# Kernel tuning notes

Measured on AMD Instinct MI355X. Metric: run time of the kernel, lower is better.

## Reference

```python
import jax, jax.numpy as jnp
import numpy as np

N_HEADS = 12

def setup_inputs() -> dict:
    key = jax.random.key(0)
    ks = jax.random.split(key, 3)
    B, C, T = 4, 768, 2048
    x = jax.random.normal(ks[0], (B, C, T), dtype=jnp.float32)
    mask = jnp.ones((B, 1, 1, T), dtype=jnp.int32)  # all valid; masked_fill where mask==0
    Wqkv = jax.random.normal(ks[1], (3 * C, C), dtype=jnp.float32) * 0.02
    bqkv = jnp.zeros((3 * C,), dtype=jnp.float32)
    Wout = jax.random.normal(ks[2], (C, C), dtype=jnp.float32) * 0.02
    bout = jnp.zeros((C,), dtype=jnp.float32)
    return {"x": x, "mask": mask, "Wqkv": Wqkv, "bqkv": bqkv, "Wout": Wout, "bout": bout}


def reference(x, mask, Wqkv, bqkv, Wout, bout):
    B, C, T = x.shape
    H = N_HEADS
    d = C // H
    scale = 1.0 / jnp.sqrt(jnp.asarray(d, x.dtype))
    # 1x1 Conv1d == per-timestep matmul over channels
    qkv = jnp.einsum('oc,bct->bot', Wqkv, x) + bqkv[None, :, None]  # [B,3C,T]
    # channel dim splits as [3, H, d] per the torch view(B,3,H,d,T)
    qkv = qkv.reshape(B, 3, H, d, T).transpose(0, 1, 2, 4, 3)       # [B,3,H,T,d]
    q, k, v = qkv[:, 0], qkv[:, 1], qkv[:, 2]
    score = jnp.einsum('bhtd,bhsd->bhts', q, k) * scale             # [B,H,T,T]
    score = jnp.where(mask == 0, jnp.asarray(-10000.0, score.dtype), score)
    attn = jax.nn.softmax(score, axis=-1)  # dropout: eval mode (identity)
    o = jnp.einsum('bhts,bhsd->bhtd', attn, v)                      # [B,H,T,d]
    o = o.transpose(0, 1, 3, 2).reshape(B, C, T)                    # [B,C,T]
    return jnp.einsum('oc,bct->bot', Wout, o) + bout[None, :, None]
```

## Files before the change

kernel.cpp:

```cpp
#include <hip/hip_runtime.h>
#include <hip/hip_bf16.h>
#include <stdint.h>

#define B_   4
#define C_   768
#define T_   2048
#define H_   12
#define D_   64
#define O3_  2304

typedef __attribute__((ext_vector_type(4))) float f32x4;
typedef __attribute__((ext_vector_type(8))) short bf16x8;

__device__ __forceinline__ unsigned short f2bf(float f) {
  union { float f; unsigned int u; } v; v.f = f;
  unsigned int r = v.u + 0x7fffu + ((v.u >> 16) & 1u);
  return (unsigned short)(r >> 16);
}

__device__ __forceinline__ unsigned int pack2bf(float a, float b) {
  __hip_bfloat162 h2 = __float22bfloat162_rn(make_float2(a, b));
  union { __hip_bfloat162 h; unsigned int u; } cv; cv.h = h2;
  return cv.u;
}

__device__ __forceinline__ float fexp2(float x) {
#if __has_builtin(__builtin_amdgcn_exp2f)
  return __builtin_amdgcn_exp2f(x);
#else
  return exp2f(x);
#endif
}

__device__ __forceinline__ void async16(const void* g, void* lds) {
#if __has_builtin(__builtin_amdgcn_global_load_lds)
  __builtin_amdgcn_global_load_lds((const __attribute__((address_space(1))) void*)g,
                                   (__attribute__((address_space(3))) void*)lds, 16, 0, 0);
#else
  int lane = threadIdx.x & 63;
  *((uint4*)((char*)lds + lane * 16)) = *((const uint4*)g);
#endif
}


__global__ void cvt_f32_bf16(const float* __restrict__ in,
                             unsigned short* __restrict__ out, int n4) {
  int i = blockIdx.x * 256 + threadIdx.x;
  if (i < n4) {
    float4 f = ((const float4*)in)[i];
    ushort4 o;
    o.x = f2bf(f.x); o.y = f2bf(f.y); o.z = f2bf(f.z); o.w = f2bf(f.w);
    ((ushort4*)out)[i] = o;
  }
}

__global__ void make_bias(const int* __restrict__ mask, float* __restrict__ mbias, int n) {
  int i = blockIdx.x * 256 + threadIdx.x;
  if (i < n) mbias[i] = (mask[i] == 0) ? -14426.950408f : 0.0f;
}

__global__ void transpose_x(const float* __restrict__ x,
                            unsigned short* __restrict__ xT) {
  __shared__ unsigned short tile[32][33];
  int b = blockIdx.z;
  int c0 = blockIdx.y * 32;
  int t0 = blockIdx.x * 32;
  int tid = threadIdx.x;
  {
    int cl = tid >> 3;
    int tl = (tid & 7) * 4;
    float4 f = *(const float4*)(x + ((size_t)b * C_ + c0 + cl) * T_ + t0 + tl);
    tile[tl + 0][cl] = f2bf(f.x);
    tile[tl + 1][cl] = f2bf(f.y);
    tile[tl + 2][cl] = f2bf(f.z);
    tile[tl + 3][cl] = f2bf(f.w);
  }
  __syncthreads();
  {
    int tl = tid >> 3;
    int cl = (tid & 7) * 4;
    ushort4 o;
    o.x = tile[tl][cl + 0]; o.y = tile[tl][cl + 1];
    o.z = tile[tl][cl + 2]; o.w = tile[tl][cl + 3];
    *(ushort4*)(xT + ((size_t)b * T_ + t0 + tl) * C_ + c0 + cl) = o;
  }
}

__global__ __launch_bounds__(256, 3)
void gemm_qkv(const unsigned short* __restrict__ xT,
              const unsigned short* __restrict__ W1,
              const float* __restrict__ bqkv,
              unsigned short* __restrict__ Qb,
              unsigned short* __restrict__ Kb,
              unsigned short* __restrict__ Vb) {
  __shared__ unsigned short sA[3][128 * 32];
  __shared__ unsigned short sB[3][128 * 32];

  const int b   = blockIdx.z;
  const int o0  = blockIdx.y * 128;
  const int t0  = blockIdx.x * 128;
  const int tid = threadIdx.x;
  const int wave = tid >> 6, lane = tid & 63;
  const int q = lane >> 4, ln = lane & 15;
  const int tw = wave >> 1, ow = wave & 1;

  const unsigned short* Ax = xT + (size_t)b * T_ * C_;
  const int srow = lane >> 2;
  const int ssw  = ((lane >> 2) ^ (lane >> 4)) & 3;
  const int scol = ((lane & 3) ^ ssw) * 8;
  const int rsw  = (ln ^ (ln >> 2)) & 3;

  const f32x4 ZERO = {0.f, 0.f, 0.f, 0.f};
  f32x4 acc[4][4];
#pragma unroll
  for (int mi = 0; mi < 4; ++mi)
#pragma unroll
    for (int ni = 0; ni < 4; ++ni) acc[mi][ni] = ZERO;

  auto stageA = [&](int ks, int bufi) {
#pragma unroll
    for (int j = 0; j < 2; ++j) {
      const int chunk = wave * 2 + j;
      async16(Ax + (size_t)(t0 + chunk * 16 + srow) * C_ + ks * 32 + scol,
              &sA[bufi][chunk * 512]);
    }
  };
  auto stageB = [&](int ks, int bufi) {
#pragma unroll
    for (int j = 0; j < 2; ++j) {
      const int chunk = wave * 2 + j;
      async16(W1 + (size_t)(o0 + chunk * 16 + srow) * C_ + ks * 32 + scol,
              &sB[bufi][chunk * 512]);
    }
  };
  auto sync4 = [&]() {
    __builtin_amdgcn_sched_barrier(0);
    asm volatile("s_waitcnt vmcnt(4) lgkmcnt(0)" ::: "memory");
    __builtin_amdgcn_s_barrier();
    __builtin_amdgcn_sched_barrier(0);
  };
  auto sync0 = [&]() {
    __builtin_amdgcn_sched_barrier(0);
    asm volatile("s_waitcnt vmcnt(0) lgkmcnt(0)" ::: "memory");
    __builtin_amdgcn_s_barrier();
    __builtin_amdgcn_sched_barrier(0);
  };
  auto compute = [&](int bufi) {
    bf16x8 aF[4], bF[4];
#pragma unroll
    for (int mi = 0; mi < 4; ++mi)
      aF[mi] = *(const bf16x8*)(&sA[bufi][(tw * 64 + mi * 16 + ln) * 32 + ((q ^ rsw) << 3)]);
#pragma unroll
    for (int ni = 0; ni < 4; ++ni)
      bF[ni] = *(const bf16x8*)(&sB[bufi][(ow * 64 + ni * 16 + ln) * 32 + ((q ^ rsw) << 3)]);
#pragma unroll
    for (int mi = 0; mi < 4; ++mi)
#pragma unroll
      for (int ni = 0; ni < 4; ++ni)
        acc[mi][ni] = __builtin_amdgcn_mfma_f32_16x16x32_bf16(aF[mi], bF[ni], acc[mi][ni], 0, 0, 0);
  };

  stageA(0, 0); stageB(0, 0);
  stageA(1, 1); stageB(1, 1);

  for (int g = 0; g < 7; ++g) {
    const int t3 = g * 3;
    sync4(); stageA(t3 + 2, 2); stageB(t3 + 2, 2); compute(0);
    sync4(); stageA(t3 + 3, 0); stageB(t3 + 3, 0); compute(1);
    sync4(); stageA(t3 + 4, 1); stageB(t3 + 4, 1); compute(2);
  }
  sync4(); stageA(23, 2); stageB(23, 2); compute(0);
  sync4(); compute(1);
  sync0(); compute(2);

  const float QSCL = 0.125f * 1.44269504f;
#pragma unroll
  for (int ni = 0; ni < 4; ++ni) {
    const int o = o0 + ow * 64 + ni * 16 + ln;
    const float bias = bqkv[o];
    const int which = o / C_;
    const int rem = o - which * C_;
    const int bh = b * H_ + (rem >> 6);
    const int dd = rem & 63;
#pragma unroll
    for (int mi = 0; mi < 4; ++mi) {
      const int tb = t0 + tw * 64 + mi * 16 + q * 4;
      f32x4 v = acc[mi][ni];
      if (which == 0) {
#pragma unroll
        for (int r = 0; r < 4; ++r)
          Qb[((size_t)bh * T_ + tb + r) * D_ + dd] = f2bf((v[r] + bias) * QSCL);
      } else if (which == 1) {
#pragma unroll
        for (int r = 0; r < 4; ++r) {
          const int s = tb + r;
          const int cp = (dd >> 3) ^ (s & 7);
          Kb[((size_t)bh * T_ + s) * 64 + (cp << 3) + (dd & 7)] = f2bf(v[r] + bias);
        }
      } else {
        const int tile = tb >> 6, si = tb & 63;
        const int cp = (si >> 3) ^ (dd & 7);
        ushort4 pk;
        pk.x = f2bf(v[0] + bias);
        pk.y = f2bf(v[1] + bias);
        pk.z = f2bf(v[2] + bias);
        pk.w = f2bf(v[3] + bias);
        *(ushort4*)(Vb + (((size_t)bh * 32 + tile) * 64 + dd) * 64 + (cp << 3) + (si & 7)) = pk;
      }
    }
  }
}

__global__ __launch_bounds__(256, 3)
void attn(const unsigned short* __restrict__ Qb,
          const unsigned short* __restrict__ Kb,
          const unsigned short* __restrict__ Vb,
          const float* __restrict__ mbias,
          unsigned short* __restrict__ Ob) {
  __shared__ __align__(16) char smem[49152];
  unsigned short* sK0 = (unsigned short*)smem;
  unsigned short* sV0 = (unsigned short*)(smem + 24576);

  const int id = blockIdx.x;
  const int bh = id % 48;
  const int tblk = id / 48;
  const int b = bh / H_, h = bh % H_;
  const int tid = threadIdx.x, wave = tid >> 6, lane = tid & 63;
  const int q = lane >> 4, ln = lane & 15;
  const int t0w = tblk * 128 + wave * 32;

  bf16x8 Qa[2][2];
#pragma unroll
  for (int tt = 0; tt < 2; ++tt) {
    const unsigned short* qrow = Qb + ((size_t)bh * T_ + t0w + tt * 16 + ln) * D_;
    Qa[tt][0] = *(const bf16x8*)(qrow + q * 8);
    Qa[tt][1] = *(const bf16x8*)(qrow + 32 + q * 8);
  }

  const f32x4 ZERO = {0.f, 0.f, 0.f, 0.f};
  f32x4 Oacc[4][2];
  f32x4 lacc[2];
#pragma unroll
  for (int dt = 0; dt < 4; ++dt)
#pragma unroll
    for (int tt = 0; tt < 2; ++tt) Oacc[dt][tt] = ZERO;
#pragma unroll
  for (int tt = 0; tt < 2; ++tt) lacc[tt] = ZERO;

  const short one_s = (ln == 0) ? (short)0x3F80 : (short)0;
  bf16x8 ones;
#pragma unroll
  for (int j = 0; j < 8; ++j) ones[j] = one_s;

  const unsigned short* gK = Kb + (size_t)bh * T_ * 64;
  const unsigned short* gV = Vb + (size_t)bh * 32 * 4096;
  const float* mb = mbias + b * T_;

  unsigned int maskbits = 0;
  for (int t2 = 0; t2 < 32; ++t2)
    if (__ballot(mb[t2 * 64 + lane] != 0.0f) != 0ull) maskbits |= (1u << t2);

  auto stage = [&](const unsigned short* g, unsigned short* lds) {
#pragma unroll
    for (int j = 0; j < 2; ++j) {
      const int chunk = wave * 2 + j;
      async16(g + chunk * 512 + lane * 8, lds + chunk * 512);
    }
  };

  auto sync4 = [&]() {
    __builtin_amdgcn_sched_barrier(0);
    asm volatile("s_waitcnt vmcnt(4) lgkmcnt(0)" ::: "memory");
    __builtin_amdgcn_s_barrier();
    __builtin_amdgcn_sched_barrier(0);
  };
  auto sync0 = [&]() {
    __builtin_amdgcn_sched_barrier(0);
    asm volatile("s_waitcnt vmcnt(0) lgkmcnt(0)" ::: "memory");
    __builtin_amdgcn_s_barrier();
    __builtin_amdgcn_sched_barrier(0);
  };

  auto QK = [&](const unsigned short* sKc, int it, bf16x8 pfO[2][2]) {
    const int s0 = it * 64;
    const bool anymask = (maskbits >> it) & 1;
#pragma unroll
    for (int kc = 0; kc < 2; ++kc) {
      bf16x8 kf0[2], kf1[2];
#pragma unroll
      for (int sb = 0; sb < 2; ++sb) {
        const unsigned short* krow = sKc + (kc * 32 + sb * 16 + ln) * 64;
        kf0[sb] = *(const bf16x8*)(krow + ((q ^ (ln & 7)) << 3));
        kf1[sb] = *(const bf16x8*)(krow + (((4 + q) ^ (ln & 7)) << 3));
      }
#pragma unroll
      for (int tt = 0; tt < 2; ++tt) {
        f32x4 sc[2];
#pragma unroll
        for (int sb = 0; sb < 2; ++sb) {
          f32x4 p0 = __builtin_amdgcn_mfma_f32_16x16x32_bf16(kf0[sb], Qa[tt][0], ZERO, 0, 0, 0);
          sc[sb]   = __builtin_amdgcn_mfma_f32_16x16x32_bf16(kf1[sb], Qa[tt][1], p0, 0, 0, 0);
          if (anymask) {
            f32x4 bb = *(const f32x4*)(mb + s0 + kc * 32 + sb * 16 + q * 4);
#pragma unroll
            for (int r = 0; r < 4; ++r) sc[sb][r] += bb[r];
          }
        }
        unsigned int A0 = pack2bf(fexp2(sc[0][0]), fexp2(sc[0][1]));
        unsigned int B0 = pack2bf(fexp2(sc[0][2]), fexp2(sc[0][3]));
        unsigned int C0 = pack2bf(fexp2(sc[1][0]), fexp2(sc[1][1]));
        unsigned int E0 = pack2bf(fexp2(sc[1][2]), fexp2(sc[1][3]));
        asm volatile("v_permlane32_swap_b32 %0, %1" : "+v"(A0), "+v"(C0));
        asm volatile("v_permlane16_swap_b32 %0, %1" : "+v"(A0), "+v"(C0));
        asm volatile("v_permlane32_swap_b32 %0, %1" : "+v"(B0), "+v"(E0));
        asm volatile("v_permlane16_swap_b32 %0, %1" : "+v"(B0), "+v"(E0));
        union { bf16x8 v; unsigned int u[4]; } P;
        P.u[0] = A0;
        P.u[1] = B0;
        P.u[2] = C0;
        P.u[3] = E0;
        pfO[tt][kc] = P.v;
      }
    }
  };

  auto PV = [&](const unsigned short* sVc, bf16x8 pfI[2][2]) {
#pragma unroll
    for (int dt = 0; dt < 4; ++dt) {
#pragma unroll
      for (int kc = 0; kc < 2; ++kc) {
        bf16x8 vf = *(const bf16x8*)(sVc + (dt * 16 + ln) * 64 +
                                     (((kc * 4 + q) ^ (ln & 7)) << 3));
#pragma unroll
        for (int tt = 0; tt < 2; ++tt)
          Oacc[dt][tt] = __builtin_amdgcn_mfma_f32_16x16x32_bf16(vf, pfI[tt][kc], Oacc[dt][tt], 0, 0, 0);
      }
    }
#pragma unroll
    for (int kc = 0; kc < 2; ++kc)
#pragma unroll
      for (int tt = 0; tt < 2; ++tt)
        lacc[tt] = __builtin_amdgcn_mfma_f32_16x16x32_bf16(ones, pfI[tt][kc], lacc[tt], 0, 0, 0);
  };

  bf16x8 pf[2][2];

  stage(gK, sK0);
  stage(gV, sV0);
  stage(gK + 4096, sK0 + 4096);
  stage(gV + 4096, sV0 + 4096);

  for (int ith = 0; ith < 10; ++ith) {
    const int it = ith * 3;
    sync4();
    stage(gK + (size_t)(it + 2) * 4096, sK0 + 2 * 4096);
    stage(gV + (size_t)(it + 2) * 4096, sV0 + 2 * 4096);
    QK(sK0, it, pf);
    PV(sV0, pf);
    sync4();
    stage(gK + (size_t)(it + 3) * 4096, sK0);
    stage(gV + (size_t)(it + 3) * 4096, sV0);
    QK(sK0 + 4096, it + 1, pf);
    PV(sV0 + 4096, pf);
    sync4();
    stage(gK + (size_t)(it + 4) * 4096, sK0 + 4096);
    stage(gV + (size_t)(it + 4) * 4096, sV0 + 4096);
    QK(sK0 + 2 * 4096, it + 2, pf);
    PV(sV0 + 2 * 4096, pf);
  }

  sync4();
  QK(sK0, 30, pf);
  PV(sV0, pf);
  sync0();
  QK(sK0 + 4096, 31, pf);
  PV(sV0 + 4096, pf);

#pragma unroll
  for (int tt = 0; tt < 2; ++tt) {
    const float lv = __shfl(lacc[tt][0], ln, 64);
    const float inv = 1.0f / lv;
    const int t = t0w + tt * 16 + ln;
#pragma unroll
    for (int dt = 0; dt < 4; ++dt) {
      f32x4 o = Oacc[dt][tt];
      ushort4 pk;
      pk.x = f2bf(o[0] * inv);
      pk.y = f2bf(o[1] * inv);
      pk.z = f2bf(o[2] * inv);
      pk.w = f2bf(o[3] * inv);
      *(ushort4*)(Ob + ((size_t)b * T_ + t) * C_ + h * D_ + dt * 16 + q * 4) = pk;
    }
  }
}

__global__ __launch_bounds__(256, 3)
void gemm_out(const unsigned short* __restrict__ Ob,
              const unsigned short* __restrict__ W2,
              const float* __restrict__ bout,
              float* __restrict__ out) {
  __shared__ unsigned short sA[3][128 * 32];
  __shared__ unsigned short sB[3][128 * 32];

  const int b   = blockIdx.z;
  const int o0  = blockIdx.y * 128;
  const int t0  = blockIdx.x * 128;
  const int tid = threadIdx.x;
  const int wave = tid >> 6, lane = tid & 63;
  const int q = lane >> 4, ln = lane & 15;
  const int tw = wave >> 1, ow = wave & 1;

  const unsigned short* Bo = Ob + (size_t)b * T_ * C_;
  const int srow = lane >> 2;
  const int ssw  = ((lane >> 2) ^ (lane >> 4)) & 3;
  const int scol = ((lane & 3) ^ ssw) * 8;
  const int rsw  = (ln ^ (ln >> 2)) & 3;

  const f32x4 ZERO = {0.f, 0.f, 0.f, 0.f};
  f32x4 acc[4][4];
#pragma unroll
  for (int mi = 0; mi < 4; ++mi)
#pragma unroll
    for (int ni = 0; ni < 4; ++ni) acc[mi][ni] = ZERO;

  auto stageA = [&](int ks, int bufi) {
#pragma unroll
    for (int j = 0; j < 2; ++j) {
      const int chunk = wave * 2 + j;
      async16(W2 + (size_t)(o0 + chunk * 16 + srow) * C_ + ks * 32 + scol,
              &sA[bufi][chunk * 512]);
    }
  };
  auto stageB = [&](int ks, int bufi) {
#pragma unroll
    for (int j = 0; j < 2; ++j) {
      const int chunk = wave * 2 + j;
      async16(Bo + (size_t)(t0 + chunk * 16 + srow) * C_ + ks * 32 + scol,
              &sB[bufi][chunk * 512]);
    }
  };
  auto sync4 = [&]() {
    __builtin_amdgcn_sched_barrier(0);
    asm volatile("s_waitcnt vmcnt(4) lgkmcnt(0)" ::: "memory");
    __builtin_amdgcn_s_barrier();
    __builtin_amdgcn_sched_barrier(0);
  };
  auto sync0 = [&]() {
    __builtin_amdgcn_sched_barrier(0);
    asm volatile("s_waitcnt vmcnt(0) lgkmcnt(0)" ::: "memory");
    __builtin_amdgcn_s_barrier();
    __builtin_amdgcn_sched_barrier(0);
  };
  auto compute = [&](int bufi) {
    bf16x8 aF[4], bF[4];
#pragma unroll
    for (int mi = 0; mi < 4; ++mi)
      aF[mi] = *(const bf16x8*)(&sA[bufi][(tw * 64 + mi * 16 + ln) * 32 + ((q ^ rsw) << 3)]);
#pragma unroll
    for (int ni = 0; ni < 4; ++ni)
      bF[ni] = *(const bf16x8*)(&sB[bufi][(ow * 64 + ni * 16 + ln) * 32 + ((q ^ rsw) << 3)]);
#pragma unroll
    for (int mi = 0; mi < 4; ++mi)
#pragma unroll
      for (int ni = 0; ni < 4; ++ni)
        acc[mi][ni] = __builtin_amdgcn_mfma_f32_16x16x32_bf16(aF[mi], bF[ni], acc[mi][ni], 0, 0, 0);
  };

  stageA(0, 0); stageB(0, 0);
  stageA(1, 1); stageB(1, 1);

  for (int g = 0; g < 7; ++g) {
    const int t3 = g * 3;
    sync4(); stageA(t3 + 2, 2); stageB(t3 + 2, 2); compute(0);
    sync4(); stageA(t3 + 3, 0); stageB(t3 + 3, 0); compute(1);
    sync4(); stageA(t3 + 4, 1); stageB(t3 + 4, 1); compute(2);
  }
  sync4(); stageA(23, 2); stageB(23, 2); compute(0);
  sync4(); compute(1);
  sync0(); compute(2);

#pragma unroll
  for (int mi = 0; mi < 4; ++mi) {
    const int ob = o0 + tw * 64 + mi * 16 + q * 4;
#pragma unroll
    for (int ni = 0; ni < 4; ++ni) {
      const int t = t0 + ow * 64 + ni * 16 + ln;
      f32x4 v = acc[mi][ni];
#pragma unroll
      for (int r = 0; r < 4; ++r)
        out[((size_t)b * C_ + ob + r) * T_ + t] = v[r] + bout[ob + r];
    }
  }
}


extern "C" void kernel_launch(void* const* d_in, const int* in_sizes, int n_in,
                              void* d_out, int out_size, void* d_ws, size_t ws_size,
                              hipStream_t stream) {
  (void)in_sizes; (void)n_in; (void)out_size; (void)ws_size;
  const float* x    = (const float*)d_in[0];
  const int*   mask = (const int*)d_in[1];
  const float* Wqkv = (const float*)d_in[2];
  const float* bqkv = (const float*)d_in[3];
  const float* Wout = (const float*)d_in[4];
  const float* bout = (const float*)d_in[5];
  float* out = (float*)d_out;

  const size_t szHead = (size_t)B_ * H_ * T_ * D_;
  const size_t szBTC  = (size_t)B_ * T_ * C_;
  unsigned short* Qb  = (unsigned short*)d_ws;
  unsigned short* Kb  = Qb + szHead;
  unsigned short* Vb  = Kb + szHead;
  unsigned short* Ob  = Vb + szHead;
  unsigned short* xT  = Ob + szBTC;
  unsigned short* W1b = xT + szBTC;
  unsigned short* W2b = W1b + (size_t)O3_ * C_;
  float* mbias        = (float*)(W2b + (size_t)C_ * C_);

  cvt_f32_bf16<<<dim3((O3_ * C_ / 4 + 255) / 256), 256, 0, stream>>>(Wqkv, W1b, O3_ * C_ / 4);
  cvt_f32_bf16<<<dim3((C_ * C_ / 4 + 255) / 256), 256, 0, stream>>>(Wout, W2b, C_ * C_ / 4);
  make_bias<<<dim3((B_ * T_ + 255) / 256), 256, 0, stream>>>(mask, mbias, B_ * T_);
  transpose_x<<<dim3(T_ / 32, C_ / 32, B_), 256, 0, stream>>>(x, xT);
  gemm_qkv<<<dim3(T_ / 128, O3_ / 128, B_), 256, 0, stream>>>(xT, W1b, bqkv, Qb, Kb, Vb);
  attn<<<dim3(768), 256, 0, stream>>>(Qb, Kb, Vb, mbias, Ob);
  gemm_out<<<dim3(T_ / 128, C_ / 128, B_), 256, 0, stream>>>(Ob, W2b, bout, out);
}
```

Before: 225.1 us.

## Stagger block starts with sleeps, prioritize MFMA waves, halve out-GEMM tile

Adds phase-dependent s_sleep at the start of the QKV GEMM, attention and output GEMM kernels, so later waves of blocks start staggered instead of all contending for memory at once. In attention, the QK and PV MFMA sections are wrapped in s_setprio(1), and the mask-bias add is moved out of the MFMA loop. The output GEMM tile is halved from 128x128 to 64x128, doubling its grid to 768 blocks for better CU fill, with fewer loads per stage and the wait count adjusted to match. The sleeps add idle cycles, and the smaller tile lowers data reuse per block.

```diff
diff --git a/kernel.cpp b/kernel.cpp
--- a/kernel.cpp
+++ b/kernel.cpp
@@ -104,6 +104,13 @@
   const int q = lane >> 4, ln = lane & 15;
   const int tw = wave >> 1, ow = wave & 1;
 
+  {
+    const int lin = blockIdx.x + 16 * (blockIdx.y + 18 * blockIdx.z);
+    const int ph = lin >> 8;
+    if (ph == 1) __builtin_amdgcn_s_sleep(5);
+    else if (ph == 2) __builtin_amdgcn_s_sleep(10);
+  }
+
   const unsigned short* Ax = xT + (size_t)b * T_ * C_;
   const int srow = lane >> 2;
   const int ssw  = ((lane >> 2) ^ (lane >> 4)) & 3;
@@ -229,6 +236,12 @@
   const int q = lane >> 4, ln = lane & 15;
   const int t0w = tblk * 128 + wave * 32;
 
+  {
+    const int ph = id >> 8;
+    if (ph == 1) __builtin_amdgcn_s_sleep(9);
+    else if (ph == 2) __builtin_amdgcn_s_sleep(18);
+  }
+
   bf16x8 Qa[2][2];
 #pragma unroll
   for (int tt = 0; tt < 2; ++tt) {
@@ -296,11 +309,16 @@
 #pragma unroll
       for (int tt = 0; tt < 2; ++tt) {
         f32x4 sc[2];
+        __builtin_amdgcn_s_setprio(1);
 #pragma unroll
         for (int sb = 0; sb < 2; ++sb) {
           f32x4 p0 = __builtin_amdgcn_mfma_f32_16x16x32_bf16(kf0[sb], Qa[tt][0], ZERO, 0, 0, 0);
           sc[sb]   = __builtin_amdgcn_mfma_f32_16x16x32_bf16(kf1[sb], Qa[tt][1], p0, 0, 0, 0);
-          if (anymask) {
+        }
+        __builtin_amdgcn_s_setprio(0);
+        if (anymask) {
+#pragma unroll
+          for (int sb = 0; sb < 2; ++sb) {
             f32x4 bb = *(const f32x4*)(mb + s0 + kc * 32 + sb * 16 + q * 4);
 #pragma unroll
             for (int r = 0; r < 4; ++r) sc[sb][r] += bb[r];
@@ -325,6 +343,7 @@
   };
 
   auto PV = [&](const unsigned short* sVc, bf16x8 pfI[2][2]) {
+    __builtin_amdgcn_s_setprio(1);
 #pragma unroll
     for (int dt = 0; dt < 4; ++dt) {
 #pragma unroll
@@ -341,6 +360,7 @@
 #pragma unroll
       for (int tt = 0; tt < 2; ++tt)
         lacc[tt] = __builtin_amdgcn_mfma_f32_16x16x32_bf16(ones, pfI[tt][kc], lacc[tt], 0, 0, 0);
+    __builtin_amdgcn_s_setprio(0);
   };
 
   bf16x8 pf[2][2];
@@ -399,17 +419,24 @@
               const unsigned short* __restrict__ W2,
               const float* __restrict__ bout,
               float* __restrict__ out) {
-  __shared__ unsigned short sA[3][128 * 32];
+  __shared__ unsigned short sA[3][64 * 32];
   __shared__ unsigned short sB[3][128 * 32];
 
   const int b   = blockIdx.z;
-  const int o0  = blockIdx.y * 128;
+  const int o0  = blockIdx.y * 64;
   const int t0  = blockIdx.x * 128;
   const int tid = threadIdx.x;
   const int wave = tid >> 6, lane = tid & 63;
   const int q = lane >> 4, ln = lane & 15;
   const int tw = wave >> 1, ow = wave & 1;
 
+  {
+    const int lin = blockIdx.x + 16 * (blockIdx.y + 12 * blockIdx.z);
+    const int ph = lin >> 8;
+    if (ph == 1) __builtin_amdgcn_s_sleep(5);
+    else if (ph == 2) __builtin_amdgcn_s_sleep(10);
+  }
+
   const unsigned short* Bo = Ob + (size_t)b * T_ * C_;
   const int srow = lane >> 2;
   const int ssw  = ((lane >> 2) ^ (lane >> 4)) & 3;
@@ -417,19 +444,15 @@
   const int rsw  = (ln ^ (ln >> 2)) & 3;
 
   const f32x4 ZERO = {0.f, 0.f, 0.f, 0.f};
-  f32x4 acc[4][4];
-#pragma unroll
-  for (int mi = 0; mi < 4; ++mi)
+  f32x4 acc[2][4];
+#pragma unroll
+  for (int mi = 0; mi < 2; ++mi)
 #pragma unroll
     for (int ni = 0; ni < 4; ++ni) acc[mi][ni] = ZERO;
 
   auto stageA = [&](int ks, int bufi) {
-#pragma unroll
-    for (int j = 0; j < 2; ++j) {
-      const int chunk = wave * 2 + j;
-      async16(W2 + (size_t)(o0 + chunk * 16 + srow) * C_ + ks * 32 + scol,
-              &sA[bufi][chunk * 512]);
-    }
+    async16(W2 + (size_t)(o0 + wave * 16 + srow) * C_ + ks * 32 + scol,
+            &sA[bufi][wave * 512]);
   };
   auto stageB = [&](int ks, int bufi) {
 #pragma unroll
@@ -439,9 +462,9 @@
               &sB[bufi][chunk * 512]);
     }
   };
-  auto sync4 = [&]() {
-    __builtin_amdgcn_sched_barrier(0);
-    asm volatile("s_waitcnt vmcnt(4) lgkmcnt(0)" ::: "memory");
+  auto sync3 = [&]() {
+    __builtin_amdgcn_sched_barrier(0);
+    asm volatile("s_waitcnt vmcnt(3) lgkmcnt(0)" ::: "memory");
     __builtin_amdgcn_s_barrier();
     __builtin_amdgcn_sched_barrier(0);
   };
@@ -452,15 +475,15 @@
     __builtin_amdgcn_sched_barrier(0);
   };
   auto compute = [&](int bufi) {
-    bf16x8 aF[4], bF[4];
-#pragma unroll
-    for (int mi = 0; mi < 4; ++mi)
-      aF[mi] = *(const bf16x8*)(&sA[bufi][(tw * 64 + mi * 16 + ln) * 32 + ((q ^ rsw) << 3)]);
+    bf16x8 aF[2], bF[4];
+#pragma unroll
+    for (int mi = 0; mi < 2; ++mi)
+      aF[mi] = *(const bf16x8*)(&sA[bufi][(tw * 32 + mi * 16 + ln) * 32 + ((q ^ rsw) << 3)]);
 #pragma unroll
     for (int ni = 0; ni < 4; ++ni)
       bF[ni] = *(const bf16x8*)(&sB[bufi][(ow * 64 + ni * 16 + ln) * 32 + ((q ^ rsw) << 3)]);
 #pragma unroll
-    for (int mi = 0; mi < 4; ++mi)
+    for (int mi = 0; mi < 2; ++mi)
 #pragma unroll
       for (int ni = 0; ni < 4; ++ni)
         acc[mi][ni] = __builtin_amdgcn_mfma_f32_16x16x32_bf16(aF[mi], bF[ni], acc[mi][ni], 0, 0, 0);
@@ -471,17 +494,17 @@
 
   for (int g = 0; g < 7; ++g) {
     const int t3 = g * 3;
-    sync4(); stageA(t3 + 2, 2); stageB(t3 + 2, 2); compute(0);
-    sync4(); stageA(t3 + 3, 0); stageB(t3 + 3, 0); compute(1);
-    sync4(); stageA(t3 + 4, 1); stageB(t3 + 4, 1); compute(2);
-  }
-  sync4(); stageA(23, 2); stageB(23, 2); compute(0);
-  sync4(); compute(1);
+    sync3(); stageA(t3 + 2, 2); stageB(t3 + 2, 2); compute(0);
+    sync3(); stageA(t3 + 3, 0); stageB(t3 + 3, 0); compute(1);
+    sync3(); stageA(t3 + 4, 1); stageB(t3 + 4, 1); compute(2);
+  }
+  sync3(); stageA(23, 2); stageB(23, 2); compute(0);
+  sync3(); compute(1);
   sync0(); compute(2);
 
 #pragma unroll
-  for (int mi = 0; mi < 4; ++mi) {
-    const int ob = o0 + tw * 64 + mi * 16 + q * 4;
+  for (int mi = 0; mi < 2; ++mi) {
+    const int ob = o0 + tw * 32 + mi * 16 + q * 4;
 #pragma unroll
     for (int ni = 0; ni < 4; ++ni) {
       const int t = t0 + ow * 64 + ni * 16 + ln;
@@ -523,5 +546,5 @@
   transpose_x<<<dim3(T_ / 32, C_ / 32, B_), 256, 0, stream>>>(x, xT);
   gemm_qkv<<<dim3(T_ / 128, O3_ / 128, B_), 256, 0, stream>>>(xT, W1b, bqkv, Qb, Kb, Vb);
   attn<<<dim3(768), 256, 0, stream>>>(Qb, Kb, Vb, mbias, Ob);
-  gemm_out<<<dim3(T_ / 128, C_ / 128, B_), 256, 0, stream>>>(Ob, W2b, bout, out);
-}
+  gemm_out<<<dim3(T_ / 128, C_ / 64, B_), 256, 0, stream>>>(Ob, W2b, bout, out);
+}
```

New measurement: 225.7 us. No clear change (+0.3%).
